# Kernel optimization log

Measured on AMD Instinct MI355X. Metric: run time of the kernel, lower is better.

## Reference

```python
import jax, jax.numpy as jnp
import numpy as np
import math

N_SAMPLES = 15


def sample_match(P, n_samples=N_SAMPLES):
    """Greedy argmax matching with row/col suppression, vectorized over batch.
    P: [B, N, M] (non-negative softmax scores). Returns (rows, cols): [B, S] int32.
    Matches torch: idx = (P == P.max()).nonzero()[0] -> first (row-major) argmax.
    """
    B, N, M = P.shape
    row_ids = jnp.arange(N)
    col_ids = jnp.arange(M)

    def step(P, _):
        flat_idx = jnp.argmax(P.reshape(B, N * M), axis=1)  # first max, row-major
        row = flat_idx // M  # [B]
        col = flat_idx % M   # [B]
        # suppress chosen row and column: P[row,:]=0 ; P[:,col]=0
        mask = (row_ids[None, :, None] == row[:, None, None]) | (
            col_ids[None, None, :] == col[:, None, None])  # [B,N,M]
        P = jnp.where(mask, jnp.zeros((), P.dtype), P)
        return P, (row, col)

    _, (rows, cols) = jax.lax.scan(step, P, None, length=n_samples)
    return rows.T, cols.T  # [B, S]


def setup_inputs() -> dict:
    key = jax.random.key(0)
    k1, k2, k3, k4 = jax.random.split(key, 4)
    B, D, N = 16, 512, 2048
    return {
        "src_embedding": jax.random.normal(k1, (B, D, N), dtype=jnp.float32),
        "tgt_embedding": jax.random.normal(k2, (B, D, N), dtype=jnp.float32),
        "src": jax.random.normal(k3, (B, N, 3), dtype=jnp.float32),
        "tgt": jax.random.normal(k4, (B, N, 3), dtype=jnp.float32),
    }


def reference(src_embedding, tgt_embedding, src, tgt):
    # input_shape == 'bnc': permute point clouds to [B, 3, N]
    src = jnp.swapaxes(src, 1, 2)
    tgt = jnp.swapaxes(tgt, 1, 2)
    B = src.shape[0]
    d_k = src_embedding.shape[1]

    # scores[b, s, t] = softmax_t( <src_emb[b,:,s], tgt_emb[b,:,t]> / sqrt(d_k) )
    logits = jnp.einsum('bds,bdt->bst', src_embedding, tgt_embedding) / math.sqrt(d_k)
    scores = jax.nn.softmax(logits, axis=2)

    # greedy one-to-one matching on detached scores
    rows, cols = sample_match(jax.lax.stop_gradient(scores))  # [B, S]

    # gather matched points: [B, 3, S]
    topk_src = jnp.take_along_axis(src, rows[:, None, :], axis=2)
    topk_tgt = jnp.take_along_axis(tgt, cols[:, None, :], axis=2)

    src_c = topk_src - topk_src.mean(axis=2, keepdims=True)
    tgt_c = topk_tgt - topk_tgt.mean(axis=2, keepdims=True)
    H = jnp.einsum('bis,bjs->bij', src_c, tgt_c)  # [B, 3, 3]

    u, s, vh = jnp.linalg.svd(H)
    v = jnp.swapaxes(vh, -1, -2)  # torch.svd returns V, jnp returns V^H
    ut = jnp.swapaxes(u, -1, -2)
    r = v @ ut
    det = jnp.linalg.det(r)
    reflect = jnp.array([1.0, 1.0, -1.0], dtype=H.dtype)  # diag(1,1,-1) right-mult
    r_fix = (v * reflect[None, None, :]) @ ut
    R = jnp.where((det < 0)[:, None, None], r_fix, r)  # [B, 3, 3]

    # soft correspondence: src_corr = tgt @ scores^T  -> [B, 3, N_src]
    src_corr = jnp.einsum('bjt,bst->bjs', tgt, scores)
    t = jnp.einsum('bij,bj->bi', -R, src.mean(axis=2)) + src_corr.mean(axis=2)
    return R, t.reshape(B, 3)
```

## Files before the change

kernel.cpp:

```cpp
#include <hip/hip_runtime.h>
#include <hip/hip_fp16.h>
#include <math.h>

typedef unsigned short u16;
typedef __attribute__((ext_vector_type(8))) short bf16x8;
typedef __attribute__((ext_vector_type(4))) float f32x4;

constexpr int B_ = 16;
constexpr int D_ = 512;
constexpr int N_ = 2048;
constexpr int S_ = 15;
constexpr int TOPK = 16;

constexpr int BK  = 32;
constexpr int KP  = 2 * D_;
constexpr int BN7 = 256;
constexpr int SCW4 = 68;
constexpr int SBUF = 24576;

__device__ __forceinline__ void gl_lds16(const void* g, void* s) {
    __builtin_amdgcn_global_load_lds(
        (const __attribute__((address_space(1))) unsigned int*)g,
        (__attribute__((address_space(3))) unsigned int*)s, 16, 0, 0);
}

__device__ __forceinline__ unsigned enc1(float x) {
    x = fminf(x, 448.f);
    unsigned u = __float_as_uint(x);
    if (u < 0x3C800000u) return 0u;
    unsigned r = u + 0x7FFFFu + ((u >> 20) & 1u);
    unsigned f = (r >> 20) - 0x3C0u;
    return f > 0x7Eu ? 0x7Eu : f;
}
__device__ __forceinline__ float dec1(unsigned f) {
    return f ? __uint_as_float((f + 0x3C0u) << 20) : 0.f;
}

__global__ __launch_bounds__(256) void packbf(
    const float* __restrict__ srcE, const float* __restrict__ tgtE,
    u16* __restrict__ srcP, u16* __restrict__ tgtP)
{
    const int t = threadIdx.x;
    const int b = blockIdx.z & 15, sel = blockIdx.z >> 4;
    const float* in = (sel ? tgtE : srcE) + (size_t)b * D_ * N_;
    u16* out = (sel ? tgtP : srcP) + (size_t)b * N_ * KP;
    const int n0 = blockIdx.x * 64, k0 = blockIdx.y * 64;

    __shared__ float T[64][69];

    #pragma unroll
    for (int it = 0; it < 4; it++) {
        int r = it * 16 + (t >> 4);
        int c = (t & 15) * 4;
        float4 v = *(const float4*)&in[(size_t)(k0 + r) * N_ + n0 + c];
        T[c + 0][r] = v.x; T[c + 1][r] = v.y; T[c + 2][r] = v.z; T[c + 3][r] = v.w;
    }
    __syncthreads();

    const int nn = t >> 2, kc = (t & 3) * 16;
    __align__(16) u16 hi[16], lo[16];
    #pragma unroll
    for (int j = 0; j < 16; j++) {
        float x = T[nn][kc + j];
        unsigned u = __float_as_uint(x);
        unsigned hr = u + 0x7fff + ((u >> 16) & 1);
        u16 h = (u16)(hr >> 16);
        float hf = __uint_as_float((unsigned)h << 16);
        float xl = x - hf;
        unsigned ul = __float_as_uint(xl);
        unsigned lr = ul + 0x7fff + ((ul >> 16) & 1);
        hi[j] = h; lo[j] = (u16)(lr >> 16);
    }
    u16* op = out + (size_t)(n0 + nn) * KP + k0 + kc;
    *(int4*)op         = *(int4*)hi;  *(int4*)(op + 8)   = *(int4*)(hi + 8);
    *(int4*)(op + 512) = *(int4*)lo;  *(int4*)(op + 520) = *(int4*)(lo + 8);
}

__global__ __launch_bounds__(512, 2) void gemm7(
    const u16* __restrict__ srcP, const u16* __restrict__ tgtP,
    float* __restrict__ rzbuf, float* __restrict__ topv, int* __restrict__ topc,
    unsigned char* __restrict__ e8)
{
    __shared__ __align__(16) u16 sS[2 * SBUF];
    __shared__ __align__(16) float sC[128 * SCW4];

    const int tid = threadIdx.x;
    const int w = tid >> 6, lane = tid & 63;
    const int wr = w >> 2, wc = w & 3;
    const int sr = lane >> 2, q = lane & 3;
    const int bid = blockIdx.x;
    const int swz = (bid & 7) * 32 + (bid >> 3);
    const int b  = swz >> 4;
    const int s0 = (swz & 15) * 128;
    const float scale = 0.044194173824159216f;

    const u16* srcPb = srcP + (size_t)b * N_ * KP;
    const u16* tgtPb = tgtP + (size_t)b * N_ * KP;

    const int sls = ((lane & 3) ^ ((lane >> 3) & 3)) * 8;
    const u16* pAh = srcPb + (size_t)(s0 + w * 16 + (lane >> 2)) * KP + sls;
    const u16* pB  = tgtPb + (size_t)(w * 16 + (lane >> 2)) * KP + sls;
    const int aro = (lane & 15) * BK + (((lane >> 4) ^ ((lane >> 1) & 3)) * 8);

    auto stage = [&](int bi, int kt, int c0) {
        u16* base = &sS[bi * SBUF];
        const int t32 = kt * BK;
        gl_lds16(pAh + t32,       base + w * 512);
        gl_lds16(pAh + 512 + t32, base + 4096 + w * 512);
        gl_lds16(pB + (size_t)c0 * KP + t32,               base + 8192  + w * 512);
        gl_lds16(pB + (size_t)(c0 + 128) * KP + t32,       base + 12288 + w * 512);
        gl_lds16(pB + (size_t)c0 * KP + 512 + t32,         base + 16384 + w * 512);
        gl_lds16(pB + (size_t)(c0 + 128) * KP + 512 + t32, base + 20480 + w * 512);
    };

    float z_loc = 0.f;
    float tv[TOPK]; int tc16[TOPK];
    #pragma unroll
    for (int k = 0; k < TOPK; k++) { tv[k] = -1e30f; tc16[k] = 0x7fffffff; }

    stage(0, 0, 0);

    for (int ch = 0; ch < 8; ch++) {
        const int c0 = ch * BN7;
        f32x4 acc[4][4];
        #pragma unroll
        for (int i = 0; i < 4; i++)
            #pragma unroll
            for (int j = 0; j < 4; j++) acc[i][j] = (f32x4){0.f, 0.f, 0.f, 0.f};

        for (int kt = 0; kt < 16; kt++) {
            __syncthreads();
            if (kt < 15)      stage((kt + 1) & 1, kt + 1, c0);
            else if (ch < 7)  stage(0, 0, c0 + BN7);
            const u16* base = &sS[(kt & 1) * SBUF];
            bf16x8 ah[4], bh[4], tf[4];
            #pragma unroll
            for (int j = 0; j < 4; j++)
                bh[j] = *(const bf16x8*)&base[8192 + wc * 2048 + j * 512 + aro];
            #pragma unroll
            for (int i = 0; i < 4; i++)
                ah[i] = *(const bf16x8*)&base[wr * 2048 + i * 512 + aro];
            #pragma unroll
            for (int i = 0; i < 4; i++)
                #pragma unroll
                for (int j = 0; j < 4; j++)
                    acc[i][j] = __builtin_amdgcn_mfma_f32_16x16x32_bf16(
                        ah[i], bh[j], acc[i][j], 0, 0, 0);
            #pragma unroll
            for (int i = 0; i < 4; i++)
                tf[i] = *(const bf16x8*)&base[4096 + wr * 2048 + i * 512 + aro];
            #pragma unroll
            for (int i = 0; i < 4; i++)
                #pragma unroll
                for (int j = 0; j < 4; j++)
                    acc[i][j] = __builtin_amdgcn_mfma_f32_16x16x32_bf16(
                        tf[i], bh[j], acc[i][j], 0, 0, 0);
            #pragma unroll
            for (int j = 0; j < 4; j++)
                tf[j] = *(const bf16x8*)&base[16384 + wc * 2048 + j * 512 + aro];
            #pragma unroll
            for (int i = 0; i < 4; i++)
                #pragma unroll
                for (int j = 0; j < 4; j++)
                    acc[i][j] = __builtin_amdgcn_mfma_f32_16x16x32_bf16(
                        ah[i], tf[j], acc[i][j], 0, 0, 0);
        }

        #pragma unroll 1
        for (int h = 0; h < 4; h++) {
            asm volatile("s_waitcnt lgkmcnt(0)" ::: "memory");
            __builtin_amdgcn_s_barrier();
            if (wc == h) {
                #pragma unroll
                for (int i = 0; i < 4; i++)
                    #pragma unroll
                    for (int j = 0; j < 4; j++)
                        #pragma unroll
                        for (int r = 0; r < 4; r++)
                            sC[(wr * 64 + i * 16 + (lane >> 4) * 4 + r) * SCW4
                               + j * 16 + (lane & 15)] = acc[i][j][r] * scale;
            }
            asm volatile("s_waitcnt lgkmcnt(0)" ::: "memory");
            __builtin_amdgcn_s_barrier();
            const float* rowp = &sC[(w * 16 + sr) * SCW4 + q * 16];
            const int cbase = c0 + h * 64 + q * 16;
            unsigned ow0 = 0, ow1 = 0, ow2 = 0, ow3 = 0;
            #pragma unroll
            for (int mi = 0; mi < 4; mi++) {
                float4 v4 = *(const float4*)&rowp[mi * 4];
                const float vv[4] = {v4.x, v4.y, v4.z, v4.w};
                unsigned wb = 0;
                #pragma unroll
                for (int e = 0; e < 4; e++) {
                    float v = vv[e];
                    float ex = __expf(v);
                    z_loc += ex;
                    wb |= enc1(ex) << (8 * e);
                    if (v > tv[15]) {
                        const int c = cbase + mi * 4 + e;
                        #pragma unroll
                        for (int k = 15; k >= 1; k--) {
                            bool bk  = v > tv[k];
                            bool bk1 = v > tv[k - 1];
                            float sv = bk1 ? tv[k - 1] : v;
                            int   sc = bk1 ? tc16[k - 1] : c;
                            tv[k]   = bk ? sv : tv[k];
                            tc16[k] = bk ? sc : tc16[k];
                        }
                        if (v > tv[0]) { tv[0] = v; tc16[0] = c; }
                    }
                }
                if (mi == 0) ow0 = wb; else if (mi == 1) ow1 = wb;
                else if (mi == 2) ow2 = wb; else ow3 = wb;
            }
            if (e8) {
                const size_t erow = ((size_t)(b * N_ + s0 + w * 16 + sr)) * N_ + cbase;
                *(uint4*)&e8[erow] = make_uint4(ow0, ow1, ow2, ow3);
            }
        }
    }

    float* sCw = (float*)sS + w * 2112;
    int*   cbw = (int*)sCw;
    float* vbw = sCw + 1024;
    float* zqw = sCw + 2048;
    zqw[lane] = z_loc;
    #pragma unroll
    for (int k = 0; k < TOPK; k++) {
        vbw[lane * 16 + k] = tv[k];
        cbw[lane * 16 + k] = tc16[k];
    }
    if (q == 0) {
        float Z = zqw[lane] + zqw[lane + 1] + zqw[lane + 2] + zqw[lane + 3];
        float lz = logf(Z);
        const int grow = s0 + w * 16 + sr;
        rzbuf[b * N_ + grow] = 1.0f / Z;
        float tmin = -1e30f; int tminslot = 0, tmincol = 0x7fffffff;
        #pragma unroll
        for (int k = 0; k < TOPK; k++) { tv[k] = -1e30f; tc16[k] = 0x7fffffff; }
        for (int qq = 0; qq < 4; qq++) {
            #pragma unroll 1
            for (int k = 0; k < TOPK; k++) {
                float v = vbw[(lane + qq) * 16 + k];
                int c = cbw[(lane + qq) * 16 + k];
                bool ins = (v > tmin) || (v == tmin && c < tmincol);
                if (ins) {
                    #pragma unroll
                    for (int k2 = 0; k2 < TOPK; k2++)
                        if (k2 == tminslot) { tv[k2] = v; tc16[k2] = c; }
                    tmin = tv[0]; tmincol = tc16[0]; tminslot = 0;
                    #pragma unroll
                    for (int k2 = 1; k2 < TOPK; k2++) {
                        bool worse = (tv[k2] < tmin) || (tv[k2] == tmin && tc16[k2] > tmincol);
                        if (worse) { tmin = tv[k2]; tmincol = tc16[k2]; tminslot = k2; }
                    }
                }
            }
        }
        unsigned used = 0;
        size_t rowbase = ((size_t)b * N_ + grow) * TOPK;
        for (int o = 0; o < TOPK; o++) {
            float bvv = -1e31f; int bcc = 0x7fffffff; int bk = 0;
            #pragma unroll
            for (int k = 0; k < TOPK; k++) {
                bool u = (used >> k) & 1u;
                bool better = !u && ((tv[k] > bvv) || (tv[k] == bvv && tc16[k] < bcc));
                if (better) { bvv = tv[k]; bcc = tc16[k]; bk = k; }
            }
            used |= 1u << bk;
            topv[rowbase + o] = bvv - lz;
            topc[rowbase + o] = bcc;
        }
    }
}

__global__ __launch_bounds__(256) void colsum3(
    const unsigned char* __restrict__ e8, const float* __restrict__ rzbuf,
    float* __restrict__ colsum)
{
    const int b = blockIdx.z, s0 = blockIdx.y * 128, t0 = blockIdx.x * 1024;
    __shared__ float srz[128];
    if (threadIdx.x < 128) srz[threadIdx.x] = rzbuf[b * N_ + s0 + threadIdx.x];
    __syncthreads();
    const int t = t0 + threadIdx.x * 4;
    const unsigned char* p = e8 + ((size_t)(b * N_ + s0)) * N_ + t;
    float a0 = 0.f, a1 = 0.f, a2 = 0.f, a3 = 0.f;
    #pragma unroll 4
    for (int s = 0; s < 128; s++) {
        unsigned v = *(const unsigned*)(p + (size_t)s * N_);
        float r = srz[s];
        a0 += dec1(v & 255u) * r;
        a1 += dec1((v >> 8) & 255u) * r;
        a2 += dec1((v >> 16) & 255u) * r;
        a3 += dec1(v >> 24) * r;
    }
    atomicAdd(&colsum[b * N_ + t + 0], a0);
    atomicAdd(&colsum[b * N_ + t + 1], a1);
    atomicAdd(&colsum[b * N_ + t + 2], a2);
    atomicAdd(&colsum[b * N_ + t + 3], a3);
}

__global__ __launch_bounds__(512, 2) void gemm8(
    const u16* __restrict__ srcP, const u16* __restrict__ tgtP,
    const float* __restrict__ rzbuf, float* __restrict__ colsum)
{
    __shared__ __align__(16) u16 sS[2 * 16384];
    __shared__ float sRZ[128];

    const int tid = threadIdx.x;
    const int w = tid >> 6, lane = tid & 63;
    const int wr = w >> 2, wc = w & 3;
    const int bid = blockIdx.x;
    const int swz = (bid & 7) * 64 + (bid >> 3);
    const int b   = swz >> 5;
    const int rb  = swz & 31;
    const int s0  = (rb & 15) * 128;
    const int cb0 = (rb >> 4) * 1024;
    const float scale = 0.044194173824159216f;

    const u16* srcPb = srcP + (size_t)b * N_ * KP;
    const u16* tgtPb = tgtP + (size_t)b * N_ * KP;

    if (tid < 128) sRZ[tid] = rzbuf[b * N_ + s0 + tid];

    const int sls = ((lane & 3) ^ ((lane >> 3) & 3)) * 8;
    const u16* pAh = srcPb + (size_t)(s0 + w * 16 + (lane >> 2)) * KP + sls;
    const u16* pB  = tgtPb + (size_t)(w * 16 + (lane >> 2)) * KP + sls;
    const int aro = (lane & 15) * BK + (((lane >> 4) ^ ((lane >> 1) & 3)) * 8);

    auto stage = [&](int bi, int s, int c0) {
        u16* base = &sS[bi * 16384];
        const int t32 = (s & 15) * BK;
        gl_lds16(pAh + t32, base + w * 512);
        if (s < 16) {
            gl_lds16(pAh + 512 + t32, base + 4096 + w * 512);
            gl_lds16(pB + (size_t)c0 * KP + t32,         base + 8192 + w * 512);
            gl_lds16(pB + (size_t)(c0 + 128) * KP + t32, base + 12288 + w * 512);
        } else {
            gl_lds16(pB + (size_t)c0 * KP + 512 + t32,         base + 8192 + w * 512);
            gl_lds16(pB + (size_t)(c0 + 128) * KP + 512 + t32, base + 12288 + w * 512);
        }
    };

    stage(0, 0, cb0);

    for (int ch = 0; ch < 4; ch++) {
        const int c0 = cb0 + ch * BN7;
        f32x4 acc[4][4];
        #pragma unroll
        for (int i = 0; i < 4; i++)
            #pragma unroll
            for (int j = 0; j < 4; j++) acc[i][j] = (f32x4){0.f, 0.f, 0.f, 0.f};

        for (int s = 0; s < 32; s++) {
            __syncthreads();
            if (s < 31)      stage((s + 1) & 1, s + 1, c0);
            else if (ch < 3) stage(0, 0, c0 + BN7);
            const u16* base = &sS[(s & 1) * 16384];
            bf16x8 afr[4], bfr[4];
            #pragma unroll
            for (int j = 0; j < 4; j++)
                bfr[j] = *(const bf16x8*)&base[8192 + wc * 2048 + j * 512 + aro];
            #pragma unroll
            for (int i = 0; i < 4; i++)
                afr[i] = *(const bf16x8*)&base[wr * 2048 + i * 512 + aro];
            #pragma unroll
            for (int i = 0; i < 4; i++)
                #pragma unroll
                for (int j = 0; j < 4; j++)
                    acc[i][j] = __builtin_amdgcn_mfma_f32_16x16x32_bf16(
                        afr[i], bfr[j], acc[i][j], 0, 0, 0);
            if (s < 16) {
                #pragma unroll
                for (int i = 0; i < 4; i++)
                    afr[i] = *(const bf16x8*)&base[4096 + wr * 2048 + i * 512 + aro];
                #pragma unroll
                for (int i = 0; i < 4; i++)
                    #pragma unroll
                    for (int j = 0; j < 4; j++)
                        acc[i][j] = __builtin_amdgcn_mfma_f32_16x16x32_bf16(
                            afr[i], bfr[j], acc[i][j], 0, 0, 0);
            }
        }

        #pragma unroll
        for (int j = 0; j < 4; j++) {
            float s = 0.f;
            #pragma unroll
            for (int i = 0; i < 4; i++)
                #pragma unroll
                for (int r = 0; r < 4; r++)
                    s += __expf(acc[i][j][r] * scale)
                         * sRZ[wr * 64 + i * 16 + (lane >> 4) * 4 + r];
            s += __shfl_xor(s, 16);
            s += __shfl_xor(s, 32);
            if (lane < 16)
                atomicAdd(&colsum[b * N_ + c0 + wc * 64 + j * 16 + lane], s);
        }
    }
}

__global__ __launch_bounds__(256) void match2(
    const float* __restrict__ topv, const int* __restrict__ topc,
    int* __restrict__ mrow, int* __restrict__ mcol)
{
    const int b = blockIdx.x, tid = threadIdx.x;
    __shared__ float bv[N_];
    __shared__ int bc[N_];
    __shared__ int sup[16];
    __shared__ float rv[256];
    __shared__ int rr[256];

    for (int r = tid; r < N_; r += 256) {
        bv[r] = topv[((size_t)b * N_ + r) * TOPK];
        bc[r] = topc[((size_t)b * N_ + r) * TOPK];
    }
    __syncthreads();

    for (int it = 0; it < S_; it++) {
        float mv = -1e30f; int mr = 0x7fffffff;
        #pragma unroll
        for (int j = 0; j < 8; j++) {
            int r = tid + j * 256;
            float v = bv[r];
            if (v > mv) { mv = v; mr = r; }
        }
        rv[tid] = mv; rr[tid] = mr;
        __syncthreads();
        for (int off = 128; off; off >>= 1) {
            if (tid < off) {
                float v2 = rv[tid + off];
                if (v2 > rv[tid] || (v2 == rv[tid] && rr[tid + off] < rr[tid])) {
                    rv[tid] = v2; rr[tid] = rr[tid + off];
                }
            }
            __syncthreads();
        }
        if (tid == 0) {
            int R = rr[0]; int C = bc[R];
            mrow[b * S_ + it] = R; mcol[b * S_ + it] = C;
            sup[it] = C;
            bv[R] = -1e30f;
        }
        __syncthreads();
        const int C = sup[it];
        for (int r = tid; r < N_; r += 256) {
            if (bc[r] == C && bv[r] > -1e29f) {
                float nv = -1e30f; int nc = 0x7fffffff;
                const float* tvp = &topv[((size_t)b * N_ + r) * TOPK];
                const int* tcp = &topc[((size_t)b * N_ + r) * TOPK];
                for (int k = 0; k < TOPK; k++) {
                    int c2 = tcp[k];
                    bool bad = false;
                    for (int qq = 0; qq <= it; qq++) bad = bad || (sup[qq] == c2);
                    if (!bad) { nv = tvp[k]; nc = c2; break; }
                }
                bv[r] = nv; bc[r] = nc;
            }
        }
        __syncthreads();
    }
}

__global__ void finish_kernel(const float* __restrict__ src,
                              const float* __restrict__ tgt,
                              const float* __restrict__ colsum,
                              const int* __restrict__ mrow,
                              const int* __restrict__ mcol,
                              float* __restrict__ out)
{
    const int b = blockIdx.x;
    const int tid = threadIdx.x;
    __shared__ float red[256];
    __shared__ float res[6];

    float ls[3] = {0, 0, 0}, lc[3] = {0, 0, 0};
    for (int n = tid; n < N_; n += 256) {
        float cs = colsum[b * N_ + n];
        #pragma unroll
        for (int j = 0; j < 3; j++) {
            ls[j] += src[(size_t)(b * N_ + n) * 3 + j];
            lc[j] += tgt[(size_t)(b * N_ + n) * 3 + j] * cs;
        }
    }
    for (int j = 0; j < 6; j++) {
        red[tid] = (j < 3) ? ls[j] : lc[j - 3];
        __syncthreads();
        for (int off = 128; off; off >>= 1) {
            if (tid < off) red[tid] += red[tid + off];
            __syncthreads();
        }
        if (tid == 0) res[j] = red[0] / (float)N_;
        __syncthreads();
    }

    if (tid == 0) {
        double ps[S_][3], pt[S_][3];
        double ms[3] = {0, 0, 0}, mt[3] = {0, 0, 0};
        for (int s = 0; s < S_; s++) {
            int r = mrow[b * S_ + s], c = mcol[b * S_ + s];
            for (int j = 0; j < 3; j++) {
                ps[s][j] = (double)src[(size_t)(b * N_ + r) * 3 + j];
                pt[s][j] = (double)tgt[(size_t)(b * N_ + c) * 3 + j];
                ms[j] += ps[s][j]; mt[j] += pt[s][j];
            }
        }
        for (int j = 0; j < 3; j++) { ms[j] /= S_; mt[j] /= S_; }
        double H[3][3] = {{0,0,0},{0,0,0},{0,0,0}};
        for (int s = 0; s < S_; s++)
            for (int i = 0; i < 3; i++)
                for (int j = 0; j < 3; j++)
                    H[i][j] += (ps[s][i] - ms[i]) * (pt[s][j] - mt[j]);

        double A[3][3], Vv[3][3] = {{1,0,0},{0,1,0},{0,0,1}};
        for (int i = 0; i < 3; i++)
            for (int j = 0; j < 3; j++) {
                double acc = 0;
                for (int k = 0; k < 3; k++) acc += H[k][i] * H[k][j];
                A[i][j] = acc;
            }
        for (int sweep = 0; sweep < 30; sweep++) {
            double off = fabs(A[0][1]) + fabs(A[0][2]) + fabs(A[1][2]);
            if (off < 1e-30) break;
            for (int pair = 0; pair < 3; pair++) {
                int p = (pair == 2) ? 1 : 0;
                int q = (pair == 0) ? 1 : 2;
                double apq = A[p][q];
                if (fabs(apq) < 1e-300) continue;
                double theta = (A[q][q] - A[p][p]) / (2.0 * apq);
                double tt = ((theta >= 0) ? 1.0 : -1.0) / (fabs(theta) + sqrt(theta * theta + 1.0));
                double cc = 1.0 / sqrt(tt * tt + 1.0);
                double ssn = tt * cc;
                for (int k = 0; k < 3; k++) {
                    double akp = A[k][p], akq = A[k][q];
                    A[k][p] = cc * akp - ssn * akq;
                    A[k][q] = ssn * akp + cc * akq;
                }
                for (int k = 0; k < 3; k++) {
                    double apk = A[p][k], aqk = A[q][k];
                    A[p][k] = cc * apk - ssn * aqk;
                    A[q][k] = ssn * apk + cc * aqk;
                }
                for (int k = 0; k < 3; k++) {
                    double vkp = Vv[k][p], vkq = Vv[k][q];
                    Vv[k][p] = cc * vkp - ssn * vkq;
                    Vv[k][q] = ssn * vkp + cc * vkq;
                }
            }
        }
        double wv[3] = {A[0][0], A[1][1], A[2][2]};
        for (int a = 0; a < 2; a++)
            for (int b2 = a + 1; b2 < 3; b2++)
                if (wv[b2] > wv[a]) {
                    double tw = wv[a]; wv[a] = wv[b2]; wv[b2] = tw;
                    for (int k = 0; k < 3; k++) {
                        double tv_ = Vv[k][a]; Vv[k][a] = Vv[k][b2]; Vv[k][b2] = tv_;
                    }
                }
        double U[3][3];
        for (int k = 0; k < 3; k++) {
            double u[3], nrm = 0;
            for (int i = 0; i < 3; i++) {
                double acc = 0;
                for (int j = 0; j < 3; j++) acc += H[i][j] * Vv[j][k];
                u[i] = acc; nrm += acc * acc;
            }
            nrm = sqrt(nrm);
            if (nrm < 1e-300) nrm = 1e-300;
            for (int i = 0; i < 3; i++) U[i][k] = u[i] / nrm;
        }
        double r[3][3];
        for (int i = 0; i < 3; i++)
            for (int j = 0; j < 3; j++) {
                double acc = 0;
                for (int k = 0; k < 3; k++) acc += Vv[i][k] * U[j][k];
                r[i][j] = acc;
            }
        double det = r[0][0] * (r[1][1] * r[2][2] - r[1][2] * r[2][1])
                   - r[0][1] * (r[1][0] * r[2][2] - r[1][2] * r[2][0])
                   + r[0][2] * (r[1][0] * r[2][1] - r[1][1] * r[2][0]);
        if (det < 0.0) {
            for (int i = 0; i < 3; i++)
                for (int j = 0; j < 3; j++)
                    r[i][j] -= 2.0 * Vv[i][2] * U[j][2];
        }
        double smean[3] = {(double)res[0], (double)res[1], (double)res[2]};
        double cmean[3] = {(double)res[3], (double)res[4], (double)res[5]};
        for (int i = 0; i < 3; i++)
            for (int j = 0; j < 3; j++)
                out[b * 9 + i * 3 + j] = (float)r[i][j];
        for (int i = 0; i < 3; i++) {
            double acc = cmean[i];
            for (int j = 0; j < 3; j++) acc -= r[i][j] * smean[j];
            out[B_ * 9 + b * 3 + i] = (float)acc;
        }
    }
}

extern "C" void kernel_launch(void* const* d_in, const int* in_sizes, int n_in,
                              void* d_out, int out_size, void* d_ws, size_t ws_size,
                              hipStream_t stream)
{
    const float* srcE = (const float*)d_in[0];
    const float* tgtE = (const float*)d_in[1];
    const float* src  = (const float*)d_in[2];
    const float* tgt  = (const float*)d_in[3];
    float* out = (float*)d_out;
    char* ws = (char*)d_ws;

    const size_t szP  = (size_t)B_ * N_ * KP * sizeof(u16);
    const size_t szE8 = (size_t)B_ * N_ * N_;
    const size_t szStats = (size_t)B_ * N_ * sizeof(float)
                         + (size_t)B_ * N_ * TOPK * sizeof(float)
                         + (size_t)B_ * N_ * TOPK * sizeof(int)
                         + (size_t)B_ * N_ * sizeof(float)
                         + 2048;
    const bool fat = ws_size >= 2 * szP + szE8 + szStats;

    u16* srcP = (u16*)ws;
    u16* tgtP = (u16*)(ws + szP);
    unsigned char* e8 = fat ? (unsigned char*)(ws + 2 * szP) : nullptr;
    size_t off = 2 * szP + (fat ? szE8 : 0);
    float* rzbuf  = (float*)(ws + off); off += (size_t)B_ * N_ * sizeof(float);
    float* topv   = (float*)(ws + off); off += (size_t)B_ * N_ * TOPK * sizeof(float);
    int*   topc   = (int*)(ws + off);   off += (size_t)B_ * N_ * TOPK * sizeof(int);
    float* colsum = (float*)(ws + off); off += (size_t)B_ * N_ * sizeof(float);
    int*   mrow   = (int*)(ws + off);   off += 1024;
    int*   mcol   = (int*)(ws + off);

    hipMemsetAsync(colsum, 0, (size_t)B_ * N_ * sizeof(float), stream);

    packbf<<<dim3(N_ / 64, D_ / 64, 2 * B_), 256, 0, stream>>>(srcE, tgtE, srcP, tgtP);
    gemm7<<<dim3(256), 512, 0, stream>>>(srcP, tgtP, rzbuf, topv, topc, e8);
    if (fat)
        colsum3<<<dim3(2, 16, 16), 256, 0, stream>>>(e8, rzbuf, colsum);
    else
        gemm8<<<dim3(512), 512, 0, stream>>>(srcP, tgtP, rzbuf, colsum);
    match2<<<B_, 256, 0, stream>>>(topv, topc, mrow, mcol);
    finish_kernel<<<B_, 256, 0, stream>>>(src, tgt, colsum, mrow, mcol, out);
}
```

Baseline: 723.5 us.

## Pack bf16 operands into pre-tiled LDS image layout for contiguous async loads

The pack kernel now writes hi/lo bf16 splits in a tile-major layout that matches the GEMM's LDS staging order, so each global_load_lds reads contiguous 1 KB chunks per wave instead of strided rows. gemm7 and gemm8 stage from this image with simple offsets. gemm8 is also restructured to match gemm7: 256 blocks over all 8 column chunks with three MFMA passes per k-step, instead of 512 blocks splitting the columns. This aims to reduce address computation and improve load coalescing, at the cost of fewer blocks in gemm8 and a transpose-style shared-memory read in the pack kernel that may cause bank conflicts.

```diff
diff --git a/kernel.cpp b/kernel.cpp
--- a/kernel.cpp
+++ b/kernel.cpp
@@ -43,7 +43,6 @@
     const int t = threadIdx.x;
     const int b = blockIdx.z & 15, sel = blockIdx.z >> 4;
     const float* in = (sel ? tgtE : srcE) + (size_t)b * D_ * N_;
-    u16* out = (sel ? tgtP : srcP) + (size_t)b * N_ * KP;
     const int n0 = blockIdx.x * 64, k0 = blockIdx.y * 64;
 
     __shared__ float T[64][69];
@@ -53,27 +52,50 @@
         int r = it * 16 + (t >> 4);
         int c = (t & 15) * 4;
         float4 v = *(const float4*)&in[(size_t)(k0 + r) * N_ + n0 + c];
-        T[c + 0][r] = v.x; T[c + 1][r] = v.y; T[c + 2][r] = v.z; T[c + 3][r] = v.w;
+        T[r][c + 0] = v.x; T[r][c + 1] = v.y; T[r][c + 2] = v.z; T[r][c + 3] = v.w;
     }
     __syncthreads();
 
-    const int nn = t >> 2, kc = (t & 3) * 16;
-    __align__(16) u16 hi[16], lo[16];
+    const int tg = t & 127, kt_i = t >> 7;
+    const int panel = n0 >> 7, wb = (n0 & 127) >> 4;
+    const int kt = (k0 >> 5) + kt_i;
+    char* outA = (char*)srcP;
+    char* outB = (char*)tgtP;
+
     #pragma unroll
-    for (int j = 0; j < 16; j++) {
-        float x = T[nn][kc + j];
-        unsigned u = __float_as_uint(x);
-        unsigned hr = u + 0x7fff + ((u >> 16) & 1);
-        u16 h = (u16)(hr >> 16);
-        float hf = __uint_as_float((unsigned)h << 16);
-        float xl = x - hf;
-        unsigned ul = __float_as_uint(xl);
-        unsigned lr = ul + 0x7fff + ((ul >> 16) & 1);
-        hi[j] = h; lo[j] = (u16)(lr >> 16);
-    }
-    u16* op = out + (size_t)(n0 + nn) * KP + k0 + kc;
-    *(int4*)op         = *(int4*)hi;  *(int4*)(op + 8)   = *(int4*)(hi + 8);
-    *(int4*)(op + 512) = *(int4*)lo;  *(int4*)(op + 520) = *(int4*)(lo + 8);
+    for (int rep = 0; rep < 2; rep++) {
+        const int g = rep * 128 + tg;
+        const int wi = g >> 6, l = g & 63;
+        const int w = wb + wi;
+        const int s = (l & 3) ^ ((l >> 3) & 3);
+        const int n_loc = wi * 16 + (l >> 2);
+        const int kb = kt_i * 32 + s * 8;
+        __align__(16) u16 hi[8], lo[8];
+        #pragma unroll
+        for (int j = 0; j < 8; j++) {
+            float x = T[kb + j][n_loc];
+            unsigned u = __float_as_uint(x);
+            unsigned hr = u + 0x7fff + ((u >> 16) & 1);
+            u16 h = (u16)(hr >> 16);
+            float hf = __uint_as_float((unsigned)h << 16);
+            float xl = x - hf;
+            unsigned ul = __float_as_uint(xl);
+            unsigned lr = ul + 0x7fff + ((ul >> 16) & 1);
+            hi[j] = h; lo[j] = (u16)(lr >> 16);
+        }
+        if (!sel) {
+            size_t base = (((size_t)(b * 16 + panel)) << 18) + ((size_t)kt << 14)
+                        + ((size_t)w << 10) + ((size_t)l << 4);
+            *(int4*)(outA + base)        = *(int4*)hi;
+            *(int4*)(outA + base + 8192) = *(int4*)lo;
+        } else {
+            size_t base = ((size_t)b << 22) + ((size_t)(panel >> 1) << 19)
+                        + ((size_t)kt << 15) + ((size_t)(panel & 1) << 13)
+                        + ((size_t)w << 10) + ((size_t)l << 4);
+            *(int4*)(outB + base)         = *(int4*)hi;
+            *(int4*)(outB + base + 16384) = *(int4*)lo;
+        }
+    }
 }
 
 __global__ __launch_bounds__(512, 2) void gemm7(
@@ -93,24 +115,23 @@
     const int b  = swz >> 4;
     const int s0 = (swz & 15) * 128;
     const float scale = 0.044194173824159216f;
-
-    const u16* srcPb = srcP + (size_t)b * N_ * KP;
-    const u16* tgtPb = tgtP + (size_t)b * N_ * KP;
-
-    const int sls = ((lane & 3) ^ ((lane >> 3) & 3)) * 8;
-    const u16* pAh = srcPb + (size_t)(s0 + w * 16 + (lane >> 2)) * KP + sls;
-    const u16* pB  = tgtPb + (size_t)(w * 16 + (lane >> 2)) * KP + sls;
+    const int l16 = lane * 16;
+
+    const char* aimg = (const char*)srcP + (((size_t)(b * 16 + (s0 >> 7))) << 18);
+    const char* bimg = (const char*)tgtP + ((size_t)b << 22);
+
     const int aro = (lane & 15) * BK + (((lane >> 4) ^ ((lane >> 1) & 3)) * 8);
 
-    auto stage = [&](int bi, int kt, int c0) {
+    auto stage = [&](int bi, int kt, int ch) {
         u16* base = &sS[bi * SBUF];
-        const int t32 = kt * BK;
-        gl_lds16(pAh + t32,       base + w * 512);
-        gl_lds16(pAh + 512 + t32, base + 4096 + w * 512);
-        gl_lds16(pB + (size_t)c0 * KP + t32,               base + 8192  + w * 512);
-        gl_lds16(pB + (size_t)(c0 + 128) * KP + t32,       base + 12288 + w * 512);
-        gl_lds16(pB + (size_t)c0 * KP + 512 + t32,         base + 16384 + w * 512);
-        gl_lds16(pB + (size_t)(c0 + 128) * KP + 512 + t32, base + 20480 + w * 512);
+        const char* astep = aimg + ((size_t)kt << 14);
+        const char* bstep = bimg + ((size_t)ch << 19) + ((size_t)kt << 15);
+        #pragma unroll
+        for (int j = 0; j < 2; j++)
+            gl_lds16(astep + ((w * 2 + j) << 10) + l16, base + (w * 2 + j) * 512);
+        #pragma unroll
+        for (int j = 0; j < 4; j++)
+            gl_lds16(bstep + ((w * 4 + j) << 10) + l16, base + 8192 + (w * 4 + j) * 512);
     };
 
     float z_loc = 0.f;
@@ -130,8 +151,8 @@
 
         for (int kt = 0; kt < 16; kt++) {
             __syncthreads();
-            if (kt < 15)      stage((kt + 1) & 1, kt + 1, c0);
-            else if (ch < 7)  stage(0, 0, c0 + BN7);
+            if (kt < 15)      stage((kt + 1) & 1, kt + 1, ch);
+            else if (ch < 7)  stage(0, 0, ch + 1);
             const u16* base = &sS[(kt & 1) * SBUF];
             bf16x8 ah[4], bh[4], tf[4];
             #pragma unroll
@@ -189,13 +210,13 @@
             for (int mi = 0; mi < 4; mi++) {
                 float4 v4 = *(const float4*)&rowp[mi * 4];
                 const float vv[4] = {v4.x, v4.y, v4.z, v4.w};
-                unsigned wb = 0;
+                unsigned wb2 = 0;
                 #pragma unroll
                 for (int e = 0; e < 4; e++) {
                     float v = vv[e];
                     float ex = __expf(v);
                     z_loc += ex;
-                    wb |= enc1(ex) << (8 * e);
+                    wb2 |= enc1(ex) << (8 * e);
                     if (v > tv[15]) {
                         const int c = cbase + mi * 4 + e;
                         #pragma unroll
@@ -210,8 +231,8 @@
                         if (v > tv[0]) { tv[0] = v; tc16[0] = c; }
                     }
                 }
-                if (mi == 0) ow0 = wb; else if (mi == 1) ow1 = wb;
-                else if (mi == 2) ow2 = wb; else ow3 = wb;
+                if (mi == 0) ow0 = wb2; else if (mi == 1) ow1 = wb2;
+                else if (mi == 2) ow2 = wb2; else ow3 = wb2;
             }
             if (e8) {
                 const size_t erow = ((size_t)(b * N_ + s0 + w * 16 + sr)) * N_ + cbase;
@@ -304,83 +325,83 @@
     const u16* __restrict__ srcP, const u16* __restrict__ tgtP,
     const float* __restrict__ rzbuf, float* __restrict__ colsum)
 {
-    __shared__ __align__(16) u16 sS[2 * 16384];
+    __shared__ __align__(16) u16 sS[2 * SBUF];
     __shared__ float sRZ[128];
 
     const int tid = threadIdx.x;
     const int w = tid >> 6, lane = tid & 63;
     const int wr = w >> 2, wc = w & 3;
     const int bid = blockIdx.x;
-    const int swz = (bid & 7) * 64 + (bid >> 3);
-    const int b   = swz >> 5;
-    const int rb  = swz & 31;
-    const int s0  = (rb & 15) * 128;
-    const int cb0 = (rb >> 4) * 1024;
+    const int swz = (bid & 7) * 32 + (bid >> 3);
+    const int b  = swz >> 4;
+    const int s0 = (swz & 15) * 128;
     const float scale = 0.044194173824159216f;
-
-    const u16* srcPb = srcP + (size_t)b * N_ * KP;
-    const u16* tgtPb = tgtP + (size_t)b * N_ * KP;
+    const int l16 = lane * 16;
+
+    const char* aimg = (const char*)srcP + (((size_t)(b * 16 + (s0 >> 7))) << 18);
+    const char* bimg = (const char*)tgtP + ((size_t)b << 22);
+    const int aro = (lane & 15) * BK + (((lane >> 4) ^ ((lane >> 1) & 3)) * 8);
 
     if (tid < 128) sRZ[tid] = rzbuf[b * N_ + s0 + tid];
 
-    const int sls = ((lane & 3) ^ ((lane >> 3) & 3)) * 8;
-    const u16* pAh = srcPb + (size_t)(s0 + w * 16 + (lane >> 2)) * KP + sls;
-    const u16* pB  = tgtPb + (size_t)(w * 16 + (lane >> 2)) * KP + sls;
-    const int aro = (lane & 15) * BK + (((lane >> 4) ^ ((lane >> 1) & 3)) * 8);
-
-    auto stage = [&](int bi, int s, int c0) {
-        u16* base = &sS[bi * 16384];
-        const int t32 = (s & 15) * BK;
-        gl_lds16(pAh + t32, base + w * 512);
-        if (s < 16) {
-            gl_lds16(pAh + 512 + t32, base + 4096 + w * 512);
-            gl_lds16(pB + (size_t)c0 * KP + t32,         base + 8192 + w * 512);
-            gl_lds16(pB + (size_t)(c0 + 128) * KP + t32, base + 12288 + w * 512);
-        } else {
-            gl_lds16(pB + (size_t)c0 * KP + 512 + t32,         base + 8192 + w * 512);
-            gl_lds16(pB + (size_t)(c0 + 128) * KP + 512 + t32, base + 12288 + w * 512);
-        }
+    auto stage = [&](int bi, int kt, int ch) {
+        u16* base = &sS[bi * SBUF];
+        const char* astep = aimg + ((size_t)kt << 14);
+        const char* bstep = bimg + ((size_t)ch << 19) + ((size_t)kt << 15);
+        #pragma unroll
+        for (int j = 0; j < 2; j++)
+            gl_lds16(astep + ((w * 2 + j) << 10) + l16, base + (w * 2 + j) * 512);
+        #pragma unroll
+        for (int j = 0; j < 4; j++)
+            gl_lds16(bstep + ((w * 4 + j) << 10) + l16, base + 8192 + (w * 4 + j) * 512);
     };
 
-    stage(0, 0, cb0);
-
-    for (int ch = 0; ch < 4; ch++) {
-        const int c0 = cb0 + ch * BN7;
+    stage(0, 0, 0);
+
+    for (int ch = 0; ch < 8; ch++) {
+        const int c0 = ch * BN7;
         f32x4 acc[4][4];
         #pragma unroll
         for (int i = 0; i < 4; i++)
             #pragma unroll
             for (int j = 0; j < 4; j++) acc[i][j] = (f32x4){0.f, 0.f, 0.f, 0.f};
 
-        for (int s = 0; s < 32; s++) {
+        for (int kt = 0; kt < 16; kt++) {
             __syncthreads();
-            if (s < 31)      stage((s + 1) & 1, s + 1, c0);
-            else if (ch < 3) stage(0, 0, c0 + BN7);
-            const u16* base = &sS[(s & 1) * 16384];
-            bf16x8 afr[4], bfr[4];
+            if (kt < 15)      stage((kt + 1) & 1, kt + 1, ch);
+            else if (ch < 7)  stage(0, 0, ch + 1);
+            const u16* base = &sS[(kt & 1) * SBUF];
+            bf16x8 ah[4], bh[4], tf[4];
             #pragma unroll
             for (int j = 0; j < 4; j++)
-                bfr[j] = *(const bf16x8*)&base[8192 + wc * 2048 + j * 512 + aro];
-            #pragma unroll
-            for (int i = 0; i < 4; i++)
-                afr[i] = *(const bf16x8*)&base[wr * 2048 + i * 512 + aro];
+                bh[j] = *(const bf16x8*)&base[8192 + wc * 2048 + j * 512 + aro];
+            #pragma unroll
+            for (int i = 0; i < 4; i++)
+                ah[i] = *(const bf16x8*)&base[wr * 2048 + i * 512 + aro];
             #pragma unroll
             for (int i = 0; i < 4; i++)
                 #pragma unroll
                 for (int j = 0; j < 4; j++)
                     acc[i][j] = __builtin_amdgcn_mfma_f32_16x16x32_bf16(
-                        afr[i], bfr[j], acc[i][j], 0, 0, 0);
-            if (s < 16) {
-                #pragma unroll
-                for (int i = 0; i < 4; i++)
-                    afr[i] = *(const bf16x8*)&base[4096 + wr * 2048 + i * 512 + aro];
-                #pragma unroll
-                for (int i = 0; i < 4; i++)
-                    #pragma unroll
-                    for (int j = 0; j < 4; j++)
-                        acc[i][j] = __builtin_amdgcn_mfma_f32_16x16x32_bf16(
-                            afr[i], bfr[j], acc[i][j], 0, 0, 0);
-            }
+                        ah[i], bh[j], acc[i][j], 0, 0, 0);
+            #pragma unroll
+            for (int i = 0; i < 4; i++)
+                tf[i] = *(const bf16x8*)&base[4096 + wr * 2048 + i * 512 + aro];
+            #pragma unroll
+            for (int i = 0; i < 4; i++)
+                #pragma unroll
+                for (int j = 0; j < 4; j++)
+                    acc[i][j] = __builtin_amdgcn_mfma_f32_16x16x32_bf16(
+                        tf[i], bh[j], acc[i][j], 0, 0, 0);
+            #pragma unroll
+            for (int j = 0; j < 4; j++)
+                tf[j] = *(const bf16x8*)&base[16384 + wc * 2048 + j * 512 + aro];
+            #pragma unroll
+            for (int i = 0; i < 4; i++)
+                #pragma unroll
+                for (int j = 0; j < 4; j++)
+                    acc[i][j] = __builtin_amdgcn_mfma_f32_16x16x32_bf16(
+                        ah[i], tf[j], acc[i][j], 0, 0, 0);
         }
 
         #pragma unroll
@@ -635,7 +656,7 @@
     if (fat)
         colsum3<<<dim3(2, 16, 16), 256, 0, stream>>>(e8, rzbuf, colsum);
     else
-        gemm8<<<dim3(512), 512, 0, stream>>>(srcP, tgtP, rzbuf, colsum);
+        gemm8<<<dim3(256), 512, 0, stream>>>(srcP, tgtP, rzbuf, colsum);
     match2<<<B_, 256, 0, stream>>>(topv, topc, mrow, mcol);
     finish_kernel<<<B_, 256, 0, stream>>>(src, tgt, colsum, mrow, mcol, out);
 }
```

Result: no change. 722.5 us (-0.1%).
